# Kernel tuning notes

Measured on AMD Instinct MI355X. Metric: run time of the kernel, lower is better.

The kernel has to match this reference:

```python
import jax, jax.numpy as jnp
import numpy as np
import math

C = 1.0
IN_FEATURES = 512
SCALE = 1.0 / math.sqrt(IN_FEATURES)  # 1/sqrt(input_size) * lr_mul, lr_mul=1
LR_MUL = 1.0
GAIN = math.sqrt(2.0)
EPS = 1e-5       # clamp epsilon used by hyptorch-style pmath
PROJ_EPS = 1e-3  # boundary epsilon for project()


def _norm(x):
    return jnp.linalg.norm(x, axis=-1, keepdims=True)


def _artanh(x):
    return jnp.arctanh(jnp.clip(x, -1.0 + EPS, 1.0 - EPS))


def _project(x, c):
    sqrt_c = c ** 0.5
    norm = jnp.maximum(_norm(x), EPS)
    maxnorm = (1.0 - PROJ_EPS) / sqrt_c
    return jnp.where(norm > maxnorm, x / norm * maxnorm, x)


def _expmap0(u, c):
    sqrt_c = c ** 0.5
    u_norm = jnp.maximum(_norm(u), EPS)
    return jnp.tanh(sqrt_c * u_norm) * u / (sqrt_c * u_norm)


def _mobius_add(x, y, c):
    x2 = jnp.sum(x * x, axis=-1, keepdims=True)
    y2 = jnp.sum(y * y, axis=-1, keepdims=True)
    xy = jnp.sum(x * y, axis=-1, keepdims=True)
    num = (1.0 + 2.0 * c * xy + c * y2) * x + (1.0 - c * x2) * y
    denom = 1.0 + 2.0 * c * xy + c * c * x2 * y2
    return num / (denom + EPS)


def _mobius_matvec(m, x, c):
    # m: [out, in], x: [N, in]
    sqrt_c = c ** 0.5
    x_norm = jnp.maximum(_norm(x), EPS)
    mx = x @ m.T  # [N, out]
    mx_norm = jnp.maximum(_norm(mx), EPS)
    res = jnp.tanh(mx_norm / x_norm * _artanh(sqrt_c * x_norm)) * mx / (mx_norm * sqrt_c)
    zero_row = jnp.all(mx == 0, axis=-1, keepdims=True)
    return jnp.where(zero_row, jnp.zeros_like(res), res)


def _mobius_scalar_mult(x, r, c):
    sqrt_c = c ** 0.5
    x_norm = jnp.maximum(_norm(x), EPS)
    return jnp.tanh(r * _artanh(sqrt_c * x_norm)) * x / (x_norm * sqrt_c)


def setup_inputs() -> dict:
    key = jax.random.key(0)
    k1, k2, k3 = jax.random.split(key, 3)
    N, D_IN, D_OUT = 131072, 512, 512
    # scale x so points lie well inside the unit Poincare ball (norm ~ 0.45)
    x = jax.random.normal(k1, (N, D_IN), dtype=jnp.float32) * 0.02
    weight = jax.random.normal(k2, (D_OUT, D_IN), dtype=jnp.float32)
    bias = jax.random.normal(k3, (D_OUT,), dtype=jnp.float32) * 0.01
    return {"x": x, "weight": weight, "bias": bias}


def reference(x, weight, bias):
    c = C
    mv = _mobius_matvec(weight * SCALE, x, c)
    b = _expmap0(bias * LR_MUL, c)
    out = _project(_mobius_add(mv, b[None, :], c), c)
    out = jax.nn.leaky_relu(out, 0.2)
    out = _mobius_scalar_mult(out, GAIN, c)
    return out
```

## Files before the change

kernel.cpp:

```cpp
#include <hip/hip_runtime.h>
#include <math.h>

#define EPSV 1e-5f
#define SCALE_W 0.0441941738241592f
#define GAIN_R 1.4142135623730951f

typedef __attribute__((ext_vector_type(8))) short bf16x8;
typedef __attribute__((ext_vector_type(4))) float f32x4;

static __device__ __forceinline__ unsigned short f2bf(float f) {
  union { float f; unsigned int u; } v; v.f = f;
  unsigned int r = v.u + 0x7FFFu + ((v.u >> 16) & 1u);
  return (unsigned short)(r >> 16);
}

#define RED16(v) { v += __shfl_xor(v, 1); v += __shfl_xor(v, 2); v += __shfl_xor(v, 4); v += __shfl_xor(v, 8); }

__global__ void bias_expmap_k(const float* __restrict__ bias, float* __restrict__ bexp,
                              float* __restrict__ y2out) {
  __shared__ float part[8];
  int t = threadIdx.x;
  float bv = bias[t];
  float s = bv * bv;
  s += __shfl_xor(s, 1);  s += __shfl_xor(s, 2);  s += __shfl_xor(s, 4);
  s += __shfl_xor(s, 8);  s += __shfl_xor(s, 16); s += __shfl_xor(s, 32);
  if ((t & 63) == 0) part[t >> 6] = s;
  __syncthreads();
  float tot = 0.f;
#pragma unroll
  for (int i = 0; i < 8; ++i) tot += part[i];
  float un = fmaxf(sqrtf(tot), EPSV);
  float th = tanhf(un);
  bexp[t] = th * bv / un;
  if (t == 0) *y2out = th * th;
}

__global__ void pack_weight_k(const float* __restrict__ w, unsigned short* __restrict__ wsB) {
  int e = blockIdx.x * 256 + threadIdx.x;
  int o = e >> 9;
  int k = e & 511;
  int ks = k >> 5, kk = k & 31;
  int lgr = kk >> 3, j = kk & 7;
  int colhi = o >> 4, l15 = o & 15;
  int dst = ((ks * 32 + colhi) * 64 + lgr * 16 + l15) * 8 + j;
  wsB[dst] = f2bf(w[e] * SCALE_W);
}

#define RB 80
#define KSB 5120
#define SMEMSZ 81920

__global__ __launch_bounds__(512, 4)
void hyp_main_k(const float* __restrict__ x, const unsigned short* __restrict__ wsB,
                const float* __restrict__ bexp, const float* __restrict__ y2p,
                float* __restrict__ out) {
  extern __shared__ char smem[];
  const int tid  = threadIdx.x;
  const int lane = tid & 63;
  const int wave = tid >> 6;
  const int l15  = lane & 15;
  const int lgr  = lane >> 4;
  const long brow = (long)blockIdx.x * 64;

  const int arow  = tid >> 3;
  const float* xptr = x + (size_t)(brow + arow) * 512 + (tid & 7) * 4;
  char* awr = smem + arow * RB + (tid & 7) * 8;

  float xss = 0.f;
  {
    float4 buf[8];
#pragma unroll
    for (int i = 0; i < 8; ++i) buf[i] = *(const float4*)(xptr + i * 32);
#pragma unroll
    for (int ks = 0; ks < 16; ++ks) {
      float4 v = buf[ks & 7];
      if (ks < 8) buf[ks & 7] = *(const float4*)(xptr + (ks + 8) * 32);
      xss += v.x * v.x + v.y * v.y + v.z * v.z + v.w * v.w;
      uint2 pk;
      pk.x = (unsigned int)f2bf(v.x) | ((unsigned int)f2bf(v.y) << 16);
      pk.y = (unsigned int)f2bf(v.z) | ((unsigned int)f2bf(v.w) << 16);
      *(uint2*)(awr + ks * KSB) = pk;
    }
  }
  __syncthreads();

  const char* ard = smem + l15 * RB + lgr * 16;
  const char* brd = (const char*)wsB + ((size_t)(wave * 4) * 64 + lane) * 16;

  f32x4 acc[4][4];
#pragma unroll
  for (int i = 0; i < 4; ++i)
#pragma unroll
    for (int j = 0; j < 4; ++j) acc[i][j] = f32x4{0.f, 0.f, 0.f, 0.f};

#pragma unroll 4
  for (int ks = 0; ks < 16; ++ks) {
    bf16x8 af[4], bfr[4];
#pragma unroll
    for (int mf = 0; mf < 4; ++mf) af[mf] = *(const bf16x8*)(ard + ks * KSB + mf * (16 * RB));
#pragma unroll
    for (int nf = 0; nf < 4; ++nf) bfr[nf] = *(const bf16x8*)(brd + (size_t)ks * 32768 + nf * 1024);
#pragma unroll
    for (int mf = 0; mf < 4; ++mf)
#pragma unroll
      for (int nf = 0; nf < 4; ++nf)
        acc[mf][nf] = __builtin_amdgcn_mfma_f32_16x16x32_bf16(af[mf], bfr[nf], acc[mf][nf], 0, 0, 0);
  }
  __syncthreads();

  float* tds = (float*)smem;
  float* xn2 = (float*)(smem + 40960);
  float* pS2 = (float*)(smem + 40960 + 256);
  float* pSB = (float*)(smem + 40960 + 2304);
  float* g12 = (float*)(smem + 40960 + 4352);
  float* pN2 = pS2;
  float* tml = pSB;

  float xs = xss;
  xs += __shfl_xor(xs, 1); xs += __shfl_xor(xs, 2); xs += __shfl_xor(xs, 4);
  if ((lane & 7) == 0) xn2[wave * 8 + (lane >> 3)] = xs;

  float bv[4];
#pragma unroll
  for (int nf = 0; nf < 4; ++nf) bv[nf] = bexp[wave * 64 + nf * 16 + l15];

#pragma unroll
  for (int mf = 0; mf < 4; ++mf)
#pragma unroll
    for (int j = 0; j < 4; ++j) {
      float s2 = 0.f, sb = 0.f;
#pragma unroll
      for (int nf = 0; nf < 4; ++nf) {
        float v = acc[mf][nf][j];
        s2 += v * v;
        sb += v * bv[nf];
      }
      RED16(s2); RED16(sb);
      if (l15 == 0) {
        int r = mf * 16 + lgr * 4 + j;
        pS2[r * 8 + wave] = s2;
        pSB[r * 8 + wave] = sb;
      }
    }
  __syncthreads();

  if (tid < 64) {
    int r = tid;
    float S2 = 0.f, SB = 0.f;
#pragma unroll
    for (int i = 0; i < 8; ++i) { S2 += pS2[r * 8 + i]; SB += pSB[r * 8 + i]; }
    float y2 = *y2p;
    float xn  = fmaxf(sqrtf(xn2[r]), EPSV);
    float mxn = fmaxf(sqrtf(S2), EPSV);
    float f = tanhf((mxn / xn) * atanhf(fminf(xn, 1.f - EPSV))) / mxn;
    float xy = f * SB;
    float x2 = f * f * S2;
    float den = 1.f + 2.f * xy + x2 * y2 + EPSV;
    float g1 = (1.f + 2.f * xy + y2) * f / den;
    float g2 = (1.f - x2) / den;
    float n1sq = g1 * g1 * S2 + 2.f * g1 * g2 * SB + g2 * g2 * y2;
    float n1 = fmaxf(sqrtf(fmaxf(n1sq, 0.f)), EPSV);
    if (n1 > 0.999f) { float s = 0.999f / n1; g1 *= s; g2 *= s; }
    g12[r * 2] = g1; g12[r * 2 + 1] = g2;
  }
  __syncthreads();

#pragma unroll
  for (int mf = 0; mf < 4; ++mf)
#pragma unroll
    for (int j = 0; j < 4; ++j) {
      int r = mf * 16 + lgr * 4 + j;
      float g1 = g12[r * 2], g2 = g12[r * 2 + 1];
      float s2 = 0.f;
#pragma unroll
      for (int nf = 0; nf < 4; ++nf) {
        float v = g1 * acc[mf][nf][j] + g2 * bv[nf];
        v = v > 0.f ? v : 0.2f * v;
        acc[mf][nf][j] = v;
        s2 += v * v;
      }
      RED16(s2);
      if (l15 == 0) pN2[r * 8 + wave] = s2;
    }
  __syncthreads();

  if (tid < 64) {
    int r = tid;
    float s2 = 0.f;
#pragma unroll
    for (int i = 0; i < 8; ++i) s2 += pN2[r * 8 + i];
    float n2 = fmaxf(sqrtf(s2), EPSV);
    tml[r] = tanhf(GAIN_R * atanhf(fminf(n2, 1.f - EPSV))) / n2;
  }
  __syncthreads();

#pragma unroll
  for (int mf = 0; mf < 4; ++mf) {
    __syncthreads();
#pragma unroll
    for (int j = 0; j < 4; ++j) {
      int rl = lgr * 4 + j;
      float tm = tml[mf * 16 + rl];
#pragma unroll
      for (int nf = 0; nf < 4; ++nf)
        tds[rl * 516 + wave * 64 + nf * 16 + l15] = tm * acc[mf][nf][j];
    }
    __syncthreads();
#pragma unroll
    for (int i = 0; i < 4; ++i) {
      int fi = i * 512 + tid;
      int row = fi >> 7, c4 = fi & 127;
      float4 v = *(const float4*)(tds + row * 516 + c4 * 4);
      *(float4*)(out + (size_t)(brow + mf * 16 + row) * 512 + c4 * 4) = v;
    }
  }
}

extern "C" void kernel_launch(void* const* d_in, const int* in_sizes, int n_in,
                              void* d_out, int out_size, void* d_ws, size_t ws_size,
                              hipStream_t stream) {
  const float* x    = (const float*)d_in[0];
  const float* w    = (const float*)d_in[1];
  const float* bias = (const float*)d_in[2];
  float* out = (float*)d_out;

  unsigned short* wsB = (unsigned short*)d_ws;
  float* bexp = (float*)((char*)d_ws + 524288);
  float* y2p  = (float*)((char*)d_ws + 524288 + 2048);

  bias_expmap_k<<<dim3(1), dim3(512), 0, stream>>>(bias, bexp, y2p);
  pack_weight_k<<<dim3(1024), dim3(256), 0, stream>>>(w, wsB);

  const int nrows = in_sizes[0] / 512;
  hyp_main_k<<<dim3(nrows / 64), dim3(512), SMEMSZ, stream>>>(x, wsB, bexp, y2p, out);
}
```

Measured before the change: 213.6 us.

## Split fused kernel into tiled double-buffered GEMM plus separate row epilogue

Replaces the single fused kernel with two kernels. A 128x128-tiled GEMM double-buffers x and the packed weight through LDS using global_load_lds and writes bf16 matvec results and the squared x norms into the output buffer. A second kernel reads them back and does the per-row hyperbolic epilogue with wave-wide reductions. The aim is better GEMM pipelining and occupancy, at the cost of an extra round trip of the intermediate through global memory and bf16 rounding of the matvec result.

```diff
diff --git a/kernel.cpp b/kernel.cpp
--- a/kernel.cpp
+++ b/kernel.cpp
@@ -7,6 +7,8 @@
 
 typedef __attribute__((ext_vector_type(8))) short bf16x8;
 typedef __attribute__((ext_vector_type(4))) float f32x4;
+typedef __attribute__((ext_vector_type(4))) unsigned int u32x4;
+typedef __attribute__((ext_vector_type(8))) unsigned short u16x8;
 
 static __device__ __forceinline__ unsigned short f2bf(float f) {
   union { float f; unsigned int u; } v; v.f = f;
@@ -14,7 +16,15 @@
   return (unsigned short)(r >> 16);
 }
 
-#define RED16(v) { v += __shfl_xor(v, 1); v += __shfl_xor(v, 2); v += __shfl_xor(v, 4); v += __shfl_xor(v, 8); }
+static __device__ __forceinline__ unsigned int cvtpk(float lo, float hi) {
+  unsigned int r;
+  asm("v_cvt_pk_bf16_f32 %0, %1, %2" : "=v"(r) : "v"(lo), "v"(hi));
+  return r;
+}
+
+#define GLD_LDS16(gsrc, ldst)                                                                      \
+  __builtin_amdgcn_global_load_lds((const __attribute__((address_space(1))) unsigned int*)(gsrc),  \
+                                   (__attribute__((address_space(3))) unsigned int*)(ldst), 16, 0, 0)
 
 __global__ void bias_expmap_k(const float* __restrict__ bias, float* __restrict__ bexp,
                               float* __restrict__ y2out) {
@@ -46,173 +56,211 @@
   wsB[dst] = f2bf(w[e] * SCALE_W);
 }
 
-#define RB 80
-#define KSB 5120
-#define SMEMSZ 81920
-
-__global__ __launch_bounds__(512, 4)
-void hyp_main_k(const float* __restrict__ x, const unsigned short* __restrict__ wsB,
-                const float* __restrict__ bexp, const float* __restrict__ y2p,
-                float* __restrict__ out) {
+#define P1_ABUF 10240
+#define P1_BOFF 20480
+#define P1_BBUF 8192
+#define P1_SMEM 36864
+
+__global__ __launch_bounds__(256, 3)
+void gemm_mx_k(const float* __restrict__ x, const unsigned short* __restrict__ wsB,
+               float* __restrict__ ob) {
   extern __shared__ char smem[];
   const int tid  = threadIdx.x;
   const int lane = tid & 63;
   const int wave = tid >> 6;
-  const int l15  = lane & 15;
-  const int lgr  = lane >> 4;
-  const long brow = (long)blockIdx.x * 64;
-
-  const int arow  = tid >> 3;
-  const float* xptr = x + (size_t)(brow + arow) * 512 + (tid & 7) * 4;
-  char* awr = smem + arow * RB + (tid & 7) * 8;
+  const int wm = wave >> 1, wn = wave & 1;
+  const int l15 = lane & 15, lgr = lane >> 4;
+  const int wid = ((blockIdx.x & 7) << 9) + (blockIdx.x >> 3);
+  const int tm = wid >> 2, tn = wid & 3;
+  const int row_l = tid >> 1;
+  const int kh    = tid & 1;
+
+  const float* xp = x + (size_t)(tm * 128 + row_l) * 512 + kh * 16;
+  char* awr = smem + row_l * 80 + kh * 32;
+  const char* ard = smem + (wm * 64 + l15) * 80 + lgr * 16;
+  const char* brd = smem + P1_BOFF + wn * 4096 + lane * 16;
+
+  f32x4 acc[4][4];
+#pragma unroll
+  for (int mf = 0; mf < 4; ++mf)
+#pragma unroll
+    for (int nf = 0; nf < 4; ++nf) acc[mf][nf] = f32x4{0.f, 0.f, 0.f, 0.f};
 
   float xss = 0.f;
+  f32x4 st[4];
+
   {
-    float4 buf[8];
-#pragma unroll
-    for (int i = 0; i < 8; ++i) buf[i] = *(const float4*)(xptr + i * 32);
-#pragma unroll
-    for (int ks = 0; ks < 16; ++ks) {
-      float4 v = buf[ks & 7];
-      if (ks < 8) buf[ks & 7] = *(const float4*)(xptr + (ks + 8) * 32);
-      xss += v.x * v.x + v.y * v.y + v.z * v.z + v.w * v.w;
-      uint2 pk;
-      pk.x = (unsigned int)f2bf(v.x) | ((unsigned int)f2bf(v.y) << 16);
-      pk.y = (unsigned int)f2bf(v.z) | ((unsigned int)f2bf(v.w) << 16);
-      *(uint2*)(awr + ks * KSB) = pk;
-    }
+#pragma unroll
+    for (int i = 0; i < 4; ++i) st[i] = *(const f32x4*)(xp + i * 4);
+    u32x4 pa, pb;
+#pragma unroll
+    for (int i = 0; i < 4; ++i) {
+      f32x4 v = st[i];
+      xss += v[0]*v[0] + v[1]*v[1] + v[2]*v[2] + v[3]*v[3];
+    }
+    pa[0] = cvtpk(st[0][0], st[0][1]); pa[1] = cvtpk(st[0][2], st[0][3]);
+    pa[2] = cvtpk(st[1][0], st[1][1]); pa[3] = cvtpk(st[1][2], st[1][3]);
+    pb[0] = cvtpk(st[2][0], st[2][1]); pb[1] = cvtpk(st[2][2], st[2][3]);
+    pb[2] = cvtpk(st[3][0], st[3][1]); pb[3] = cvtpk(st[3][2], st[3][3]);
+    *(u32x4*)(awr) = pa;
+    *(u32x4*)(awr + 16) = pb;
+    const char* bs = (const char*)wsB + tn * 8192;
+    GLD_LDS16(bs + tid * 16, smem + P1_BOFF + tid * 16);
+    GLD_LDS16(bs + 4096 + tid * 16, smem + P1_BOFF + 4096 + tid * 16);
   }
   __syncthreads();
 
-  const char* ard = smem + l15 * RB + lgr * 16;
-  const char* brd = (const char*)wsB + ((size_t)(wave * 4) * 64 + lane) * 16;
-
-  f32x4 acc[4][4];
-#pragma unroll
-  for (int i = 0; i < 4; ++i)
-#pragma unroll
-    for (int j = 0; j < 4; ++j) acc[i][j] = f32x4{0.f, 0.f, 0.f, 0.f};
-
-#pragma unroll 4
-  for (int ks = 0; ks < 16; ++ks) {
-    bf16x8 af[4], bfr[4];
-#pragma unroll
-    for (int mf = 0; mf < 4; ++mf) af[mf] = *(const bf16x8*)(ard + ks * KSB + mf * (16 * RB));
-#pragma unroll
-    for (int nf = 0; nf < 4; ++nf) bfr[nf] = *(const bf16x8*)(brd + (size_t)ks * 32768 + nf * 1024);
-#pragma unroll
-    for (int mf = 0; mf < 4; ++mf)
+#pragma unroll 1
+  for (int t = 0; t < 16; ++t) {
+    const int cur = t & 1, nxt = cur ^ 1;
+    if (t < 15) {
+      const char* bs = (const char*)wsB + (size_t)(t + 1) * 32768 + tn * 8192;
+      char* bd = smem + P1_BOFF + nxt * P1_BBUF;
+      GLD_LDS16(bs + tid * 16, bd + tid * 16);
+      GLD_LDS16(bs + 4096 + tid * 16, bd + 4096 + tid * 16);
+      const float* p = xp + (t + 1) * 32;
+#pragma unroll
+      for (int i = 0; i < 4; ++i) st[i] = *(const f32x4*)(p + i * 4);
+    }
+    {
+      bf16x8 xf[4], wf[4];
+#pragma unroll
+      for (int mf = 0; mf < 4; ++mf)
+        xf[mf] = *(const bf16x8*)(ard + cur * P1_ABUF + mf * 1280);
 #pragma unroll
       for (int nf = 0; nf < 4; ++nf)
-        acc[mf][nf] = __builtin_amdgcn_mfma_f32_16x16x32_bf16(af[mf], bfr[nf], acc[mf][nf], 0, 0, 0);
+        wf[nf] = *(const bf16x8*)(brd + cur * P1_BBUF + nf * 1024);
+#pragma unroll
+      for (int mf = 0; mf < 4; ++mf)
+#pragma unroll
+        for (int nf = 0; nf < 4; ++nf)
+          acc[mf][nf] = __builtin_amdgcn_mfma_f32_16x16x32_bf16(wf[nf], xf[mf], acc[mf][nf], 0, 0, 0);
+    }
+    __syncthreads();
+    if (t < 15) {
+      u32x4 pa, pb;
+#pragma unroll
+      for (int i = 0; i < 4; ++i) {
+        f32x4 v = st[i];
+        xss += v[0]*v[0] + v[1]*v[1] + v[2]*v[2] + v[3]*v[3];
+      }
+      pa[0] = cvtpk(st[0][0], st[0][1]); pa[1] = cvtpk(st[0][2], st[0][3]);
+      pa[2] = cvtpk(st[1][0], st[1][1]); pa[3] = cvtpk(st[1][2], st[1][3]);
+      pb[0] = cvtpk(st[2][0], st[2][1]); pb[1] = cvtpk(st[2][2], st[2][3]);
+      pb[2] = cvtpk(st[3][0], st[3][1]); pb[3] = cvtpk(st[3][2], st[3][3]);
+      char* aw = awr + nxt * P1_ABUF;
+      *(u32x4*)(aw) = pa;
+      *(u32x4*)(aw + 16) = pb;
+    }
+    __syncthreads();
   }
-  __syncthreads();
-
-  float* tds = (float*)smem;
-  float* xn2 = (float*)(smem + 40960);
-  float* pS2 = (float*)(smem + 40960 + 256);
-  float* pSB = (float*)(smem + 40960 + 2304);
-  float* g12 = (float*)(smem + 40960 + 4352);
-  float* pN2 = pS2;
-  float* tml = pSB;
-
-  float xs = xss;
-  xs += __shfl_xor(xs, 1); xs += __shfl_xor(xs, 2); xs += __shfl_xor(xs, 4);
-  if ((lane & 7) == 0) xn2[wave * 8 + (lane >> 3)] = xs;
-
-  float bv[4];
-#pragma unroll
-  for (int nf = 0; nf < 4; ++nf) bv[nf] = bexp[wave * 64 + nf * 16 + l15];
-
+
+  unsigned short* mxu = (unsigned short*)ob;
+  const long rowb = (long)tm * 128 + wm * 64;
+  const int colb = tn * 128 + wn * 64;
 #pragma unroll
   for (int mf = 0; mf < 4; ++mf)
 #pragma unroll
-    for (int j = 0; j < 4; ++j) {
-      float s2 = 0.f, sb = 0.f;
-#pragma unroll
-      for (int nf = 0; nf < 4; ++nf) {
-        float v = acc[mf][nf][j];
-        s2 += v * v;
-        sb += v * bv[nf];
-      }
-      RED16(s2); RED16(sb);
-      if (l15 == 0) {
-        int r = mf * 16 + lgr * 4 + j;
-        pS2[r * 8 + wave] = s2;
-        pSB[r * 8 + wave] = sb;
-      }
-    }
-  __syncthreads();
-
-  if (tid < 64) {
-    int r = tid;
-    float S2 = 0.f, SB = 0.f;
-#pragma unroll
-    for (int i = 0; i < 8; ++i) { S2 += pS2[r * 8 + i]; SB += pSB[r * 8 + i]; }
-    float y2 = *y2p;
-    float xn  = fmaxf(sqrtf(xn2[r]), EPSV);
-    float mxn = fmaxf(sqrtf(S2), EPSV);
-    float f = tanhf((mxn / xn) * atanhf(fminf(xn, 1.f - EPSV))) / mxn;
-    float xy = f * SB;
-    float x2 = f * f * S2;
-    float den = 1.f + 2.f * xy + x2 * y2 + EPSV;
-    float g1 = (1.f + 2.f * xy + y2) * f / den;
-    float g2 = (1.f - x2) / den;
-    float n1sq = g1 * g1 * S2 + 2.f * g1 * g2 * SB + g2 * g2 * y2;
-    float n1 = fmaxf(sqrtf(fmaxf(n1sq, 0.f)), EPSV);
-    if (n1 > 0.999f) { float s = 0.999f / n1; g1 *= s; g2 *= s; }
-    g12[r * 2] = g1; g12[r * 2 + 1] = g2;
-  }
-  __syncthreads();
-
-#pragma unroll
-  for (int mf = 0; mf < 4; ++mf)
-#pragma unroll
-    for (int j = 0; j < 4; ++j) {
-      int r = mf * 16 + lgr * 4 + j;
-      float g1 = g12[r * 2], g2 = g12[r * 2 + 1];
-      float s2 = 0.f;
-#pragma unroll
-      for (int nf = 0; nf < 4; ++nf) {
-        float v = g1 * acc[mf][nf][j] + g2 * bv[nf];
-        v = v > 0.f ? v : 0.2f * v;
-        acc[mf][nf][j] = v;
-        s2 += v * v;
-      }
-      RED16(s2);
-      if (l15 == 0) pN2[r * 8 + wave] = s2;
-    }
-  __syncthreads();
-
-  if (tid < 64) {
-    int r = tid;
-    float s2 = 0.f;
-#pragma unroll
-    for (int i = 0; i < 8; ++i) s2 += pN2[r * 8 + i];
-    float n2 = fmaxf(sqrtf(s2), EPSV);
-    tml[r] = tanhf(GAIN_R * atanhf(fminf(n2, 1.f - EPSV))) / n2;
-  }
-  __syncthreads();
-
-#pragma unroll
-  for (int mf = 0; mf < 4; ++mf) {
-    __syncthreads();
-#pragma unroll
-    for (int j = 0; j < 4; ++j) {
-      int rl = lgr * 4 + j;
-      float tm = tml[mf * 16 + rl];
-#pragma unroll
-      for (int nf = 0; nf < 4; ++nf)
-        tds[rl * 516 + wave * 64 + nf * 16 + l15] = tm * acc[mf][nf][j];
-    }
-    __syncthreads();
-#pragma unroll
-    for (int i = 0; i < 4; ++i) {
-      int fi = i * 512 + tid;
-      int row = fi >> 7, c4 = fi & 127;
-      float4 v = *(const float4*)(tds + row * 516 + c4 * 4);
-      *(float4*)(out + (size_t)(brow + mf * 16 + row) * 512 + c4 * 4) = v;
-    }
+    for (int nf = 0; nf < 4; ++nf) {
+      uint2 pk;
+      pk.x = cvtpk(acc[mf][nf][0], acc[mf][nf][1]);
+      pk.y = cvtpk(acc[mf][nf][2], acc[mf][nf][3]);
+      *(uint2*)(mxu + (size_t)(rowb + mf * 16 + l15) * 1024 + colb + nf * 16 + lgr * 4) = pk;
+    }
+  float xs = xss + __shfl_xor(xss, 1);
+  if (tn == 0 && kh == 0)
+    ob[(size_t)(tm * 128 + row_l) * 512 + 256] = xs;
+}
+
+#define BFLY(v) { v += __shfl_xor(v, 1); v += __shfl_xor(v, 2); v += __shfl_xor(v, 4); \
+                  v += __shfl_xor(v, 8); v += __shfl_xor(v, 16); v += __shfl_xor(v, 32); }
+
+__global__ __launch_bounds__(256, 8)
+void hyp_epi_k(float* __restrict__ ob, const float* __restrict__ bexp,
+               const float* __restrict__ y2p) {
+  const int lane = threadIdx.x & 63;
+  const int wave = threadIdx.x >> 6;
+  const long rbase = (long)blockIdx.x * 64;
+  f32x4 be0 = *(const f32x4*)(bexp + lane * 8);
+  f32x4 be1 = *(const f32x4*)(bexp + lane * 8 + 4);
+  const float y2v = *y2p;
+
+#pragma unroll 1
+  for (int it = 0; it < 8; ++it) {
+    const long r0 = rbase + it * 8 + wave * 2;
+    const u16x8 m0 = *(const u16x8*)((const unsigned short*)ob + r0 * 1024 + lane * 8);
+    const u16x8 m1 = *(const u16x8*)((const unsigned short*)ob + (r0 + 1) * 1024 + lane * 8);
+    const float xq0 = ob[r0 * 512 + 256];
+    const float xq1 = ob[(r0 + 1) * 512 + 256];
+
+    float a0[8], a1[8];
+#pragma unroll
+    for (int j = 0; j < 8; ++j) {
+      union { unsigned int u; float f; } c0, c1;
+      c0.u = ((unsigned int)(unsigned short)m0[j]) << 16;
+      c1.u = ((unsigned int)(unsigned short)m1[j]) << 16;
+      a0[j] = c0.f; a1[j] = c1.f;
+    }
+    float bv[8] = {be0[0], be0[1], be0[2], be0[3], be1[0], be1[1], be1[2], be1[3]};
+
+    float s20 = 0.f, sb0 = 0.f, s21 = 0.f, sb1 = 0.f;
+#pragma unroll
+    for (int j = 0; j < 8; ++j) {
+      s20 += a0[j] * a0[j];  sb0 += a0[j] * bv[j];
+      s21 += a1[j] * a1[j];  sb1 += a1[j] * bv[j];
+    }
+    BFLY(s20); BFLY(sb0); BFLY(s21); BFLY(sb1);
+
+    float g1a, g2a, g1b, g2b;
+    {
+      float xn  = fmaxf(sqrtf(xq0), EPSV);
+      float mxn = fmaxf(sqrtf(s20), EPSV);
+      float f = tanhf((mxn / xn) * atanhf(fminf(xn, 1.f - EPSV))) / mxn;
+      float xy = f * sb0, x2 = f * f * s20;
+      float den = 1.f + 2.f * xy + x2 * y2v + EPSV;
+      g1a = (1.f + 2.f * xy + y2v) * f / den;
+      g2a = (1.f - x2) / den;
+      float n1sq = g1a * g1a * s20 + 2.f * g1a * g2a * sb0 + g2a * g2a * y2v;
+      float n1 = fmaxf(sqrtf(fmaxf(n1sq, 0.f)), EPSV);
+      if (n1 > 0.999f) { float sc = 0.999f / n1; g1a *= sc; g2a *= sc; }
+    }
+    {
+      float xn  = fmaxf(sqrtf(xq1), EPSV);
+      float mxn = fmaxf(sqrtf(s21), EPSV);
+      float f = tanhf((mxn / xn) * atanhf(fminf(xn, 1.f - EPSV))) / mxn;
+      float xy = f * sb1, x2 = f * f * s21;
+      float den = 1.f + 2.f * xy + x2 * y2v + EPSV;
+      g1b = (1.f + 2.f * xy + y2v) * f / den;
+      g2b = (1.f - x2) / den;
+      float n1sq = g1b * g1b * s21 + 2.f * g1b * g2b * sb1 + g2b * g2b * y2v;
+      float n1 = fmaxf(sqrtf(fmaxf(n1sq, 0.f)), EPSV);
+      if (n1 > 0.999f) { float sc = 0.999f / n1; g1b *= sc; g2b *= sc; }
+    }
+
+    float v0[8], v1[8], n20 = 0.f, n21 = 0.f;
+#pragma unroll
+    for (int j = 0; j < 8; ++j) {
+      float u0 = g1a * a0[j] + g2a * bv[j];
+      float u1 = g1b * a1[j] + g2b * bv[j];
+      u0 = u0 > 0.f ? u0 : 0.2f * u0;
+      u1 = u1 > 0.f ? u1 : 0.2f * u1;
+      v0[j] = u0; v1[j] = u1;
+      n20 += u0 * u0; n21 += u1 * u1;
+    }
+    BFLY(n20); BFLY(n21);
+    float nn0 = fmaxf(sqrtf(n20), EPSV);
+    float nn1 = fmaxf(sqrtf(n21), EPSV);
+    float tm0 = tanhf(GAIN_R * atanhf(fminf(nn0, 1.f - EPSV))) / nn0;
+    float tm1 = tanhf(GAIN_R * atanhf(fminf(nn1, 1.f - EPSV))) / nn1;
+
+    f32x4 o00 = {tm0 * v0[0], tm0 * v0[1], tm0 * v0[2], tm0 * v0[3]};
+    f32x4 o01 = {tm0 * v0[4], tm0 * v0[5], tm0 * v0[6], tm0 * v0[7]};
+    f32x4 o10 = {tm1 * v1[0], tm1 * v1[1], tm1 * v1[2], tm1 * v1[3]};
+    f32x4 o11 = {tm1 * v1[4], tm1 * v1[5], tm1 * v1[6], tm1 * v1[7]};
+    *(f32x4*)(ob + r0 * 512 + lane * 8)           = o00;
+    *(f32x4*)(ob + r0 * 512 + lane * 8 + 4)       = o01;
+    *(f32x4*)(ob + (r0 + 1) * 512 + lane * 8)     = o10;
+    *(f32x4*)(ob + (r0 + 1) * 512 + lane * 8 + 4) = o11;
   }
 }
 
@@ -231,6 +279,6 @@
   bias_expmap_k<<<dim3(1), dim3(512), 0, stream>>>(bias, bexp, y2p);
   pack_weight_k<<<dim3(1024), dim3(256), 0, stream>>>(w, wsB);
 
-  const int nrows = in_sizes[0] / 512;
-  hyp_main_k<<<dim3(nrows / 64), dim3(512), SMEMSZ, stream>>>(x, wsB, bexp, y2p, out);
-}
+  gemm_mx_k<<<dim3(4096), dim3(256), P1_SMEM, stream>>>(x, wsB, out);
+  hyp_epi_k<<<dim3(2048), dim3(256), 0, stream>>>(out, bexp, y2p);
+}
```

Result: slower. 295.3 us (+38.2%).
